# Optimization experiments

Hardware: AMD Instinct MI355X
Metric: run time of the kernel (lower is better)

The kernel has to match this reference:

```python
import jax, jax.numpy as jnp
import numpy as np

EMBED_DIM = 256; N_HEADS = 8; HEAD_DIM = 32; N_PAIRS = 16
POS_DIM = 2; N_LEVELS = 4; NBH = [3, 5, 7, 9]
N_Q = 2048; BATCH = 2; FULL = 128
SPATIAL_THETA = 100.0; LEVEL_THETA = 10.0
LN_EPS = 1e-5


def _grids():
    offs, lvls = [], []
    for l, s in enumerate(NBH):
        ax = np.arange(s)
        g = np.stack(np.meshgrid(ax, ax, indexing='ij'), -1).reshape(-1, 2)
        offs.append(g - (s - 1) // 2)
        lvls.append(np.full(s * s, l))
    return (np.concatenate(offs).astype(np.int32), np.concatenate(lvls).astype(np.int32))

OFFSETS, LEVEL_IDS = _grids()  # [164,2], [164]
K_PER_Q = OFFSETS.shape[0]


def _apply_rope(x, pos, freqs):
    # x: [..., n_heads, n_pairs, 2]; pos: [..., 3]; freqs: [3, n_pairs]
    ang = pos @ freqs                      # [..., n_pairs]
    c = jnp.cos(ang)[..., None, :]         # broadcast over heads
    s = jnp.sin(ang)[..., None, :]
    x1, x2 = x[..., 0], x[..., 1]
    return jnp.stack([x1 * c - x2 * s, x1 * s + x2 * c], axis=-1)


def setup_inputs() -> dict:
    key = jax.random.key(0)
    ks = jax.random.split(key, 8)
    scale = EMBED_DIM ** -0.5
    i = jnp.arange(N_PAIRS, dtype=jnp.float32) / N_PAIRS
    rope_freqs = jnp.stack([SPATIAL_THETA ** -i, SPATIAL_THETA ** -i, LEVEL_THETA ** -i])  # [3,16]
    level_spatial_shapes = jnp.array([[FULL >> l, FULL >> l] for l in range(N_LEVELS)], jnp.int32)
    return {
        'query': jax.random.normal(ks[0], (N_Q, EMBED_DIM), jnp.float32),
        'query_spatial_positions': jax.random.uniform(ks[1], (N_Q, POS_DIM), jnp.float32) * (FULL - 1),
        'stacked_feature_maps': jax.random.normal(ks[2], (BATCH, N_LEVELS, FULL, FULL, EMBED_DIM), jnp.float32) * 0.02,
        'norm_w': jnp.ones((EMBED_DIM,), jnp.float32),
        'norm_b': jnp.zeros((EMBED_DIM,), jnp.float32),
        'q_w': jax.random.normal(ks[3], (EMBED_DIM, EMBED_DIM), jnp.float32) * scale,
        'k_w': jax.random.normal(ks[4], (EMBED_DIM, EMBED_DIM), jnp.float32) * scale,
        'v_w': jax.random.normal(ks[5], (EMBED_DIM, EMBED_DIM), jnp.float32) * scale,
        'out_w': jax.random.normal(ks[6], (EMBED_DIM, EMBED_DIM), jnp.float32) * scale,
        'rope_freqs': rope_freqs,
        'query_batch_offsets': jnp.array([0, N_Q // 2, N_Q], jnp.int32),
        'level_spatial_shapes': level_spatial_shapes,
    }


def reference(query, query_spatial_positions, stacked_feature_maps, norm_w, norm_b,
              q_w, k_w, v_w, out_w, rope_freqs, query_batch_offsets, level_spatial_shapes):
    n_q = query.shape[0]
    residual = query

    # pre-LayerNorm
    mu = query.mean(-1, keepdims=True)
    var = query.var(-1, keepdims=True)
    x = (query - mu) * jax.lax.rsqrt(var + LN_EPS) * norm_w + norm_b

    # query projection + RoPE (spatial dims + level dim; queries sit at max-res level 0)
    q = x @ q_w
    qpos = jnp.concatenate([query_spatial_positions, jnp.zeros((n_q, 1), query.dtype)], -1)  # [n_q,3]
    q_rot = _apply_rope(q.reshape(n_q, N_HEADS, N_PAIRS, 2), qpos, rope_freqs).reshape(n_q, N_HEADS, HEAD_DIM)

    # multilevel neighborhood indices
    shapes_f = level_spatial_shapes.astype(query.dtype)               # [L,2]
    scaling = shapes_f / shapes_f.max(0)                              # [L,2]
    scaled = query_spatial_positions[:, None, :] * scaling[None]      # [n_q,L,2]
    centers = jnp.floor(scaled).astype(jnp.int32)                     # [n_q,L,2]
    lvl = jnp.asarray(LEVEL_IDS)                                      # [K]
    idx = centers[:, lvl, :] + jnp.asarray(OFFSETS)[None]             # [n_q,K,2]
    lsh = level_spatial_shapes[lvl]                                   # [K,2]
    valid = jnp.all((idx >= 0) & (idx < lsh[None]), -1)               # [n_q,K]
    idxc = jnp.clip(idx, 0, lsh[None] - 1)

    # per-query batch ids from offsets
    b = jnp.searchsorted(query_batch_offsets, jnp.arange(n_q, dtype=query_batch_offsets.dtype), side='right') - 1

    # sparse gather of key/value features (unspecified -> zero)
    feats = stacked_feature_maps[b[:, None], lvl[None, :], idxc[..., 0], idxc[..., 1]]  # [n_q,K,E]
    feats = feats * valid[..., None].astype(feats.dtype)

    k = feats @ k_w
    v = feats @ v_w

    # key positions at full scale + level coordinate
    stride = (shapes_f.max(0)[None] / shapes_f)[lvl]                  # [K,2]
    kpos_sp = (idx.astype(query.dtype) + 0.5) * stride[None]          # [n_q,K,2]
    kpos = jnp.concatenate([kpos_sp, jnp.broadcast_to(lvl.astype(query.dtype), (n_q, K_PER_Q))[..., None]], -1)
    k_rot = _apply_rope(k.reshape(n_q, K_PER_Q, N_HEADS, N_PAIRS, 2), kpos, rope_freqs)
    k_rot = k_rot.reshape(n_q, K_PER_Q, N_HEADS, HEAD_DIM)

    # attention over the 164 gathered keys per query
    logits = jnp.einsum('nhd,nkhd->nhk', q_rot, k_rot) / np.sqrt(HEAD_DIM)
    logits = jnp.where(valid[:, None, :], logits, jnp.asarray(-1e9, logits.dtype))
    attn = jax.nn.softmax(logits, axis=-1)
    out = jnp.einsum('nhk,nkhd->nhd', attn, v.reshape(n_q, K_PER_Q, N_HEADS, HEAD_DIM))
    out = out.reshape(n_q, EMBED_DIM) @ out_w
    return out + residual
```

## Files before the change

### kernel.cpp

```cpp
#include <hip/hip_runtime.h>
#include <hip/hip_bf16.h>

typedef unsigned short u16;
typedef short short8 __attribute__((ext_vector_type(8)));
typedef float f32x4 __attribute__((ext_vector_type(4)));

#define ROWS_PER_BATCH 21760
#define TOT_ROWS 43520

__device__ __forceinline__ u16 f2bf(float f){
  unsigned u = __builtin_bit_cast(unsigned, f);
  u += 0x7FFFu + ((u >> 16) & 1u);
  return (u16)(u >> 16);
}
__device__ __forceinline__ float bf2f(u16 h){
  return __builtin_bit_cast(float, ((unsigned)h) << 16);
}
__device__ __forceinline__ float bflo(unsigned u){ return __builtin_bit_cast(float, u << 16); }
__device__ __forceinline__ float bfhi(unsigned u){ return __builtin_bit_cast(float, u & 0xFFFF0000u); }
__device__ __forceinline__ unsigned pk2bf(float a, float b){
  __hip_bfloat162 h = __float22bfloat162_rn(make_float2(a, b));
  union { __hip_bfloat162 h2; unsigned u; } cv; cv.h2 = h; return cv.u;
}

__global__ __launch_bounds__(256) void prep_kernel(
    const float* __restrict__ qw, const float* __restrict__ kw,
    const float* __restrict__ vw, const float* __restrict__ ow,
    const float* __restrict__ q, const float* __restrict__ nw,
    const float* __restrict__ nb,
    u16* __restrict__ wtq, u16* __restrict__ wtk,
    u16* __restrict__ wtv, u16* __restrict__ wto, u16* __restrict__ x){
  const int bx = blockIdx.x;
  const int t = threadIdx.x;
  if (bx < 128){
    int e = bx * 256 + t;
    int which = e >> 13;
    int r = e & 8191;
    int cg = r >> 9;
    int kk = (r >> 6) & 7;
    int lane = r & 63;
    int quad = lane >> 4, mn = lane & 15;
    const float* s = which == 0 ? qw : which == 1 ? kw : which == 2 ? vw : ow;
    u16* d       = which == 0 ? wtq : which == 1 ? wtk : which == 2 ? wtv : wto;
    const float* base = s + (kk * 32 + quad * 8) * 256 + cg * 16 + mn;
    float e8[8];
    #pragma unroll
    for (int j = 0; j < 8; ++j) e8[j] = base[j * 256];
    uint4 o = { pk2bf(e8[0], e8[1]), pk2bf(e8[2], e8[3]),
                pk2bf(e8[4], e8[5]), pk2bf(e8[6], e8[7]) };
    *(uint4*)(d + (size_t)r * 8) = o;
  } else {
    const int row = (bx - 128) * 4 + (t >> 6);
    const int lane = t & 63;
    const float4 v = *(const float4*)(q + (size_t)row * 256 + lane * 4);
    float s1 = v.x + v.y + v.z + v.w;
    float s2 = v.x*v.x + v.y*v.y + v.z*v.z + v.w*v.w;
    #pragma unroll
    for (int o = 32; o > 0; o >>= 1){
      s1 += __shfl_xor(s1, o);
      s2 += __shfl_xor(s2, o);
    }
    float mu = s1 * (1.0f / 256.0f);
    float var = s2 * (1.0f / 256.0f) - mu * mu;
    float rs = rsqrtf(var + 1e-5f);
    const float4 wv = *(const float4*)(nw + lane * 4);
    const float4 bv = *(const float4*)(nb + lane * 4);
    float o0 = (v.x - mu) * rs * wv.x + bv.x;
    float o1 = (v.y - mu) * rs * wv.y + bv.y;
    float o2 = (v.z - mu) * rs * wv.z + bv.z;
    float o3 = (v.w - mu) * rs * wv.w + bv.w;
    uint2 pk = { pk2bf(o0, o1), pk2bf(o2, o3) };
    *(uint2*)(x + (size_t)row * 256 + lane * 4) = pk;
  }
}

__global__ __launch_bounds__(64, 4) void kv_gemm(const float* __restrict__ fm,
        const u16* __restrict__ wtkp, const u16* __restrict__ wtvp,
        const float* __restrict__ rope,
        u16* __restrict__ krot, u16* __restrict__ vmap){
  __shared__ float slab[16][66];
  __shared__ unsigned sh_cs[16][16];

  const int lane = threadIdx.x;
  const int row0 = blockIdx.x * 16;

  const int b = row0 / ROWS_PER_BATCH;
  const int rr = row0 - b * ROWS_PER_BATCH;
  int l, loff;
  if (rr < 16384)      { l = 0; loff = 0; }
  else if (rr < 20480) { l = 1; loff = 16384; }
  else if (rr < 21504) { l = 2; loff = 20480; }
  else                 { l = 3; loff = 21504; }
  const int logW = 7 - l;
  const int Wm1 = (128 >> l) - 1;
  const int cell0 = rr - loff;
  const float* fmbase = fm + (size_t)(b * 4 + l) * (128 * 128 * 256);

  const int mn = lane & 15;
  const int quad = lane >> 4;

  short8 af[8];
  {
    int cell = cell0 + mn;
    int y = cell >> logW, x = cell & Wm1;
    const float* arow = fmbase + (((y << 7) + x) << 8) + quad * 8;
    #pragma unroll
    for (int kk = 0; kk < 8; ++kk){
      float4 a0 = *(const float4*)(arow + kk * 32);
      float4 a1 = *(const float4*)(arow + kk * 32 + 4);
      union { short8 s; uint4 u; } cv;
      cv.u = (uint4){ pk2bf(a0.x, a0.y), pk2bf(a0.z, a0.w),
                      pk2bf(a1.x, a1.y), pk2bf(a1.z, a1.w) };
      af[kk] = cv.s;
    }
  }

  #pragma unroll
  for (int i = 0; i < 4; ++i){
    int id = i * 64 + lane;
    int lr = id >> 4, p = id & 15;
    int cell = cell0 + lr;
    int i0 = cell >> logW;
    int i1 = cell & Wm1;
    float fs = (float)(1 << l);
    float kx = ((float)i0 + 0.5f) * fs;
    float ky = ((float)i1 + 0.5f) * fs;
    float ang = kx * rope[p] + ky * rope[16 + p] + (float)l * rope[32 + p];
    sh_cs[lr][p] = pk2bf(__cosf(ang), __sinf(ang));
  }

  for (int m = 0; m < 2; ++m){
    const u16* wtp = m ? wtvp : wtkp;
    u16* outp = m ? vmap : krot;
    for (int cs2 = 0; cs2 < 4; ++cs2){
      const u16* wb = wtp + (size_t)((cs2 * 4 * 8) * 64 + lane) * 8;
      short8 bc[4], bn[4];
      #pragma unroll
      for (int tl = 0; tl < 4; ++tl)
        bc[tl] = *(const short8*)(wb + (size_t)(tl * 8) * 64 * 8);
      f32x4 acc[4];
      #pragma unroll
      for (int i = 0; i < 4; ++i) acc[i] = (f32x4){0.f, 0.f, 0.f, 0.f};
      #pragma unroll
      for (int kk = 0; kk < 8; ++kk){
        if (kk < 7){
          #pragma unroll
          for (int tl = 0; tl < 4; ++tl)
            bn[tl] = *(const short8*)(wb + (size_t)(tl * 8 + kk + 1) * 64 * 8);
        }
        #pragma unroll
        for (int tl = 0; tl < 4; ++tl)
          acc[tl] = __builtin_amdgcn_mfma_f32_16x16x32_bf16(af[kk], bc[tl], acc[tl], 0, 0, 0);
        #pragma unroll
        for (int tl = 0; tl < 4; ++tl) bc[tl] = bn[tl];
      }
      #pragma unroll
      for (int tl = 0; tl < 4; ++tl)
        #pragma unroll
        for (int r = 0; r < 4; ++r)
          slab[quad * 4 + r][tl * 16 + mn] = acc[tl][r];
      #pragma unroll
      for (int i = 0; i < 8; ++i){
        int pi = i * 64 + lane;
        int row = pi >> 5;
        int pl = pi & 31;
        float2 kv2 = *(const float2*)&slab[row][pl * 2];
        unsigned o;
        if (m == 0){
          unsigned csn = sh_cs[row][pl & 15];
          float c = bflo(csn), s = bfhi(csn);
          o = pk2bf(kv2.x * c - kv2.y * s, kv2.x * s + kv2.y * c);
        } else {
          o = pk2bf(kv2.x, kv2.y);
        }
        *(unsigned*)(outp + (size_t)(row0 + row) * 256 + cs2 * 64 + pl * 2) = o;
      }
    }
  }
}

__global__ __launch_bounds__(256) void gemm_xw(const u16* __restrict__ A,
        const u16* __restrict__ wt, const float* __restrict__ resid,
        float* __restrict__ out){
  const int t = threadIdx.x;
  const int row0 = blockIdx.x * 16;
  const int wv = t >> 6;
  const int lane = t & 63;
  const int mn = lane & 15;
  const int quad = lane >> 4;
  const int cg = blockIdx.y * 4 + wv;

  short8 af[8];
  {
    const u16* arow = A + (size_t)(row0 + mn) * 256 + quad * 8;
    #pragma unroll
    for (int kk = 0; kk < 8; ++kk)
      af[kk] = *(const short8*)(arow + kk * 32);
  }
  const u16* wb = wt + (size_t)((cg * 8) * 64 + lane) * 8;
  short8 bc = *(const short8*)wb;
  f32x4 acc = (f32x4){0.f, 0.f, 0.f, 0.f};
  #pragma unroll
  for (int kk = 0; kk < 8; ++kk){
    short8 bn;
    if (kk < 7) bn = *(const short8*)(wb + (size_t)(kk + 1) * 64 * 8);
    acc = __builtin_amdgcn_mfma_f32_16x16x32_bf16(af[kk], bc, acc, 0, 0, 0);
    bc = bn;
  }
  const int col = cg * 16 + mn;
  #pragma unroll
  for (int r = 0; r < 4; ++r){
    int row = row0 + quad * 4 + r;
    float val = acc[r];
    if (resid) val += resid[(size_t)row * 256 + col];
    out[(size_t)row * 256 + col] = val;
  }
}

__global__ __launch_bounds__(256) void attn3(
    const float* __restrict__ qraw, const float* __restrict__ qsp,
    const float* __restrict__ rope, const int* __restrict__ qbo, int nbo,
    const u16* __restrict__ krot, const u16* __restrict__ vmap,
    u16* __restrict__ ao){
  __shared__ float sh_q[4][8][33];
  __shared__ float sh_lg[4][168][8];
  __shared__ int   sh_row[4][168];
  __shared__ float sh_inv[4][8];
  const int t = threadIdx.x;
  const int w = t >> 6;
  const int lane = t & 63;
  const int qi = blockIdx.x * 4 + w;

  int bidx = 0;
  for (int j = 1; j < nbo; ++j) if (qi >= qbo[j]) bidx = j;
  const float p0 = qsp[qi * 2 + 0];
  const float p1 = qsp[qi * 2 + 1];

  #pragma unroll
  for (int it = 0; it < 4; ++it){
    int d = it * 64 + lane;
    float qv = qraw[(size_t)qi * 256 + d];
    int p = (d & 31) >> 1;
    float ang = p0 * rope[p] + p1 * rope[16 + p];
    float c = __cosf(ang), s = __sinf(ang);
    float partner = __shfl_xor(qv, 1);
    float val = (d & 1) ? (partner * s + qv * c) : (qv * c - partner * s);
    sh_q[w][d >> 5][d & 31] = val * 0.17677669529663687f;
  }

  #pragma unroll
  for (int it = 0; it < 3; ++it){
    int kk = it * 64 + lane;
    if (kk < 164){
      int l, dy, dx, loff;
      if (kk < 9)       { l = 0; int j = kk;      dy = j / 3 - 1; dx = j % 3 - 1; loff = 0; }
      else if (kk < 34) { l = 1; int j = kk - 9;  dy = j / 5 - 2; dx = j % 5 - 2; loff = 16384; }
      else if (kk < 83) { l = 2; int j = kk - 34; dy = j / 7 - 3; dx = j % 7 - 3; loff = 20480; }
      else              { l = 3; int j = kk - 83; dy = j / 9 - 4; dx = j % 9 - 4; loff = 21504; }
      float sc = 1.0f / (float)(1 << l);
      int i0 = (int)floorf(p0 * sc) + dy;
      int i1 = (int)floorf(p1 * sc) + dx;
      int W = 128 >> l;
      sh_row[w][kk] = (i0 < 0 || i0 >= W || i1 < 0 || i1 >= W)
                ? -1 : bidx * ROWS_PER_BATCH + loff + (i0 << (7 - l)) + i1;
    }
  }

  const int h = lane & 7;
  const int ksub = lane >> 3;
  float qreg[32];
  #pragma unroll
  for (int j = 0; j < 32; ++j) qreg[j] = sh_q[w][h][j];
  for (int pass = 0; pass < 21; ++pass){
    int kk = pass * 8 + ksub;
    if (kk < 164){
      int row = sh_row[w][kk];
      float lg = -1e9f;
      if (row >= 0){
        const uint4* kp = (const uint4*)(krot + (size_t)row * 256 + h * 32);
        uint4 A0 = kp[0], A1 = kp[1], A2 = kp[2], A3 = kp[3];
        unsigned uu[16];
        uu[0]=A0.x; uu[1]=A0.y; uu[2]=A0.z; uu[3]=A0.w;
        uu[4]=A1.x; uu[5]=A1.y; uu[6]=A1.z; uu[7]=A1.w;
        uu[8]=A2.x; uu[9]=A2.y; uu[10]=A2.z; uu[11]=A2.w;
        uu[12]=A3.x; uu[13]=A3.y; uu[14]=A3.z; uu[15]=A3.w;
        float s0 = 0.f, s1 = 0.f, s2 = 0.f, s3 = 0.f;
        #pragma unroll
        for (int j = 0; j < 4; ++j){
          s0 += qreg[2*j]      * bflo(uu[j])      + qreg[2*j+1]  * bfhi(uu[j]);
          s1 += qreg[2*j+8]    * bflo(uu[j+4])    + qreg[2*j+9]  * bfhi(uu[j+4]);
          s2 += qreg[2*j+16]   * bflo(uu[j+8])    + qreg[2*j+17] * bfhi(uu[j+8]);
          s3 += qreg[2*j+24]   * bflo(uu[j+12])   + qreg[2*j+25] * bfhi(uu[j+12]);
        }
        lg = (s0 + s1) + (s2 + s3);
      }
      sh_lg[w][kk][h] = lg;
    }
  }

  float mx = -1e30f;
  for (int kk = ksub; kk < 164; kk += 8) mx = fmaxf(mx, sh_lg[w][kk][h]);
  #pragma unroll
  for (int o = 8; o < 64; o <<= 1) mx = fmaxf(mx, __shfl_xor(mx, o));
  float ssum = 0.f;
  for (int kk = ksub; kk < 164; kk += 8){
    float e = __expf(sh_lg[w][kk][h] - mx);
    sh_lg[w][kk][h] = e;
    ssum += e;
  }
  #pragma unroll
  for (int o = 8; o < 64; o <<= 1) ssum += __shfl_xor(ssum, o);
  if (ksub == 0) sh_inv[w][h] = 1.0f / ssum;

  const int c = lane & 31;
  const int p2 = lane >> 5;
  const int hh = c >> 2;
  float a[8] = {0.f,0.f,0.f,0.f,0.f,0.f,0.f,0.f};
  #pragma unroll 4
  for (int ii = 0; ii < 82; ++ii){
    int kk = ii * 2 + p2;
    int row = sh_row[w][kk];
    int rc = row < 0 ? 0 : row;
    uint4 vv = *(const uint4*)(vmap + (size_t)rc * 256 + c * 8);
    float e = sh_lg[w][kk][hh];
    a[0] += e * bflo(vv.x); a[1] += e * bfhi(vv.x);
    a[2] += e * bflo(vv.y); a[3] += e * bfhi(vv.y);
    a[4] += e * bflo(vv.z); a[5] += e * bfhi(vv.z);
    a[6] += e * bflo(vv.w); a[7] += e * bfhi(vv.w);
  }
  #pragma unroll
  for (int j = 0; j < 8; ++j) a[j] += __shfl_xor(a[j], 32);
  if (p2 == 0){
    float inv = sh_inv[w][hh];
    uint4 o = { pk2bf(a[0]*inv, a[1]*inv), pk2bf(a[2]*inv, a[3]*inv),
                pk2bf(a[4]*inv, a[5]*inv), pk2bf(a[6]*inv, a[7]*inv) };
    *(uint4*)(ao + (size_t)qi * 256 + c * 8) = o;
  }
}

extern "C" void kernel_launch(void* const* d_in, const int* in_sizes, int n_in,
                              void* d_out, int out_size, void* d_ws, size_t ws_size,
                              hipStream_t stream) {
  (void)n_in; (void)out_size; (void)ws_size;
  const float* query  = (const float*)d_in[0];
  const float* qsp    = (const float*)d_in[1];
  const float* fm     = (const float*)d_in[2];
  const float* norm_w = (const float*)d_in[3];
  const float* norm_b = (const float*)d_in[4];
  const float* q_w    = (const float*)d_in[5];
  const float* k_w    = (const float*)d_in[6];
  const float* v_w    = (const float*)d_in[7];
  const float* out_w  = (const float*)d_in[8];
  const float* rope   = (const float*)d_in[9];
  const int*   qbo    = (const int*)d_in[10];
  float* out = (float*)d_out;
  const int n_q = in_sizes[0] / 256;
  const int nbo = in_sizes[10];

  char* p = (char*)d_ws;
  u16* krot = (u16*)p;                       p += (size_t)TOT_ROWS * 256 * 2;
  u16* vmap = (u16*)p;                       p += (size_t)TOT_ROWS * 256 * 2;
  float* qraw = (float*)p;                   p += (size_t)n_q * 256 * 4;
  u16* xbf = (u16*)p;                        p += (size_t)n_q * 256 * 2;
  u16* wtq = (u16*)p;                        p += 65536 * 2;
  u16* wtk = (u16*)p;                        p += 65536 * 2;
  u16* wtv = (u16*)p;                        p += 65536 * 2;
  u16* wto = (u16*)p;
  u16* ao = xbf;

  hipLaunchKernelGGL(prep_kernel, dim3(128 + n_q / 4), dim3(256), 0, stream,
                     q_w, k_w, v_w, out_w, query, norm_w, norm_b,
                     wtq, wtk, wtv, wto, xbf);
  hipLaunchKernelGGL(kv_gemm, dim3(TOT_ROWS / 16), dim3(64), 0, stream,
                     fm, wtk, wtv, rope, krot, vmap);
  hipLaunchKernelGGL(gemm_xw, dim3(n_q / 16, 4), dim3(256), 0, stream,
                     xbf, wtq, (const float*)nullptr, qraw);
  hipLaunchKernelGGL(attn3, dim3(n_q / 4), dim3(256), 0, stream,
                     qraw, qsp, rope, qbo, nbo, krot, vmap, ao);
  hipLaunchKernelGGL(gemm_xw, dim3(n_q / 16, 4), dim3(256), 0, stream,
                     ao, wto, query, out);
}
```

Before: 270.8 us.

## Sort queries by Morton order and remap attention blocks per XCD for locality

Adds a single-block bitonic sort kernel that orders queries by batch and the Morton code of their spatial position, producing a permutation. The attention kernel reads its query index through this permutation and remaps block IDs so that consecutive spatially-near queries land on the same XCD. Neighbouring queries then share gathered K/V rows in that XCD's L2. The cost is an extra serial single-workgroup launch. The code also assumes n_q is at most 4096 and that query indices fit in 12 bits.

New measurement: 299.6 us. 1.11x slower.

```diff
diff --git a/kernel.cpp b/kernel.cpp
--- a/kernel.cpp
+++ b/kernel.cpp
@@ -7,6 +7,7 @@
 
 #define ROWS_PER_BATCH 21760
 #define TOT_ROWS 43520
+#define MAXQ 4096
 
 __device__ __forceinline__ u16 f2bf(float f){
   unsigned u = __builtin_bit_cast(unsigned, f);
@@ -74,6 +75,45 @@
   }
 }
 
+__global__ __launch_bounds__(1024) void sort_q(
+    const float* __restrict__ qsp, const int* __restrict__ qbo, int nbo,
+    int n_q, u16* __restrict__ perm){
+  __shared__ unsigned key[MAXQ];
+  const int t = threadIdx.x;
+  int NP = 1; while (NP < n_q) NP <<= 1;
+  for (int i = t; i < NP; i += 1024){
+    unsigned k = 0xFFFFFFFFu;
+    if (i < n_q){
+      int b = 0;
+      for (int j = 1; j < nbo; ++j) if (i >= qbo[j]) b = j;
+      int x = ((int)qsp[i * 2])     & 127;
+      int y = ((int)qsp[i * 2 + 1]) & 127;
+      unsigned m = 0;
+      #pragma unroll
+      for (int bi = 0; bi < 7; ++bi)
+        m |= (((unsigned)(x >> bi) & 1u) << (2 * bi + 1))
+           | (((unsigned)(y >> bi) & 1u) << (2 * bi));
+      k = ((unsigned)b << 26) | (m << 12) | (unsigned)i;
+    }
+    key[i] = k;
+  }
+  __syncthreads();
+  for (int ks = 2; ks <= NP; ks <<= 1){
+    for (int j = ks >> 1; j > 0; j >>= 1){
+      for (int i = t; i < NP; i += 1024){
+        int p = i ^ j;
+        if (p > i){
+          unsigned a = key[i], bk = key[p];
+          bool up = (i & ks) == 0;
+          if ((up && a > bk) || (!up && a < bk)){ key[i] = bk; key[p] = a; }
+        }
+      }
+      __syncthreads();
+    }
+  }
+  for (int i = t; i < n_q; i += 1024) perm[i] = (u16)(key[i] & 4095u);
+}
+
 __global__ __launch_bounds__(64, 4) void kv_gemm(const float* __restrict__ fm,
         const u16* __restrict__ wtkp, const u16* __restrict__ wtvp,
         const float* __restrict__ rope,
@@ -220,6 +260,7 @@
 __global__ __launch_bounds__(256) void attn3(
     const float* __restrict__ qraw, const float* __restrict__ qsp,
     const float* __restrict__ rope, const int* __restrict__ qbo, int nbo,
+    const u16* __restrict__ perm,
     const u16* __restrict__ krot, const u16* __restrict__ vmap,
     u16* __restrict__ ao){
   __shared__ float sh_q[4][8][33];
@@ -229,7 +270,14 @@
   const int t = threadIdx.x;
   const int w = t >> 6;
   const int lane = t & 63;
-  const int qi = blockIdx.x * 4 + w;
+
+  const int nwg = gridDim.x;
+  const int orig = blockIdx.x;
+  const int xcd = orig & 7;
+  const int q8 = nwg >> 3, r8 = nwg & 7;
+  const int wg = (xcd < r8 ? xcd * (q8 + 1) : r8 * (q8 + 1) + (xcd - r8) * q8)
+               + (orig >> 3);
+  const int qi = perm[wg * 4 + w];
 
   int bidx = 0;
   for (int j = 1; j < nbo; ++j) if (qi >= qbo[j]) bidx = j;
@@ -365,18 +413,21 @@
   u16* wtq = (u16*)p;                        p += 65536 * 2;
   u16* wtk = (u16*)p;                        p += 65536 * 2;
   u16* wtv = (u16*)p;                        p += 65536 * 2;
-  u16* wto = (u16*)p;
+  u16* wto = (u16*)p;                        p += 65536 * 2;
+  u16* qperm = (u16*)p;
   u16* ao = xbf;
 
   hipLaunchKernelGGL(prep_kernel, dim3(128 + n_q / 4), dim3(256), 0, stream,
                      q_w, k_w, v_w, out_w, query, norm_w, norm_b,
                      wtq, wtk, wtv, wto, xbf);
+  hipLaunchKernelGGL(sort_q, dim3(1), dim3(1024), 0, stream,
+                     qsp, qbo, nbo, n_q, qperm);
   hipLaunchKernelGGL(kv_gemm, dim3(TOT_ROWS / 16), dim3(64), 0, stream,
                      fm, wtk, wtv, rope, krot, vmap);
   hipLaunchKernelGGL(gemm_xw, dim3(n_q / 16, 4), dim3(256), 0, stream,
                      xbf, wtq, (const float*)nullptr, qraw);
   hipLaunchKernelGGL(attn3, dim3(n_q / 4), dim3(256), 0, stream,
-                     qraw, qsp, rope, qbo, nbo, krot, vmap, ao);
+                     qraw, qsp, rope, qbo, nbo, qperm, krot, vmap, ao);
   hipLaunchKernelGGL(gemm_xw, dim3(n_q / 16, 4), dim3(256), 0, stream,
                      ao, wto, query, out);
 }
```

## Share staged weight tiles in LDS across four waves in kv_gemm

Applied to the files above, without the earlier changes.

The kv_gemm kernel now runs 256-thread blocks of four waves, each handling 16 rows. Each 64-column weight slice is staged cooperatively into shared memory once per block instead of being read from global memory by every wave. This cuts redundant weight traffic and L2 pressure by four times. In exchange it adds two block barriers per column slice, removes the register prefetch of the B operand, and uses about 32KB of extra LDS, which may limit occupancy.

Result: faster. 255.6 us (-5.6%).

```diff
diff --git a/kernel.cpp b/kernel.cpp
--- a/kernel.cpp
+++ b/kernel.cpp
@@ -74,15 +74,18 @@
   }
 }
 
-__global__ __launch_bounds__(64, 4) void kv_gemm(const float* __restrict__ fm,
+__global__ __launch_bounds__(256, 2) void kv_gemm(const float* __restrict__ fm,
         const u16* __restrict__ wtkp, const u16* __restrict__ wtvp,
         const float* __restrict__ rope,
         u16* __restrict__ krot, u16* __restrict__ vmap){
-  __shared__ float slab[16][66];
-  __shared__ unsigned sh_cs[16][16];
-
-  const int lane = threadIdx.x;
-  const int row0 = blockIdx.x * 16;
+  __shared__ u16 bstage[32 * 512];
+  __shared__ float slab[4][16][66];
+  __shared__ unsigned sh_cs[4][16][16];
+
+  const int t = threadIdx.x;
+  const int w = t >> 6;
+  const int lane = t & 63;
+  const int row0 = blockIdx.x * 64 + w * 16;
 
   const int b = row0 / ROWS_PER_BATCH;
   const int rr = row0 - b * ROWS_PER_BATCH;
@@ -126,48 +129,47 @@
     float kx = ((float)i0 + 0.5f) * fs;
     float ky = ((float)i1 + 0.5f) * fs;
     float ang = kx * rope[p] + ky * rope[16 + p] + (float)l * rope[32 + p];
-    sh_cs[lr][p] = pk2bf(__cosf(ang), __sinf(ang));
+    sh_cs[w][lr][p] = pk2bf(__cosf(ang), __sinf(ang));
   }
 
   for (int m = 0; m < 2; ++m){
     const u16* wtp = m ? wtvp : wtkp;
     u16* outp = m ? vmap : krot;
     for (int cs2 = 0; cs2 < 4; ++cs2){
-      const u16* wb = wtp + (size_t)((cs2 * 4 * 8) * 64 + lane) * 8;
-      short8 bc[4], bn[4];
-      #pragma unroll
-      for (int tl = 0; tl < 4; ++tl)
-        bc[tl] = *(const short8*)(wb + (size_t)(tl * 8) * 64 * 8);
+      __syncthreads();
+      const u16* src = wtp + (size_t)cs2 * 16384;
+      #pragma unroll
+      for (int i = 0; i < 8; ++i)
+        *(uint4*)(bstage + ((size_t)(i * 256 + t)) * 8) =
+            *(const uint4*)(src + ((size_t)(i * 256 + t)) * 8);
+      __syncthreads();
+
       f32x4 acc[4];
       #pragma unroll
       for (int i = 0; i < 4; ++i) acc[i] = (f32x4){0.f, 0.f, 0.f, 0.f};
       #pragma unroll
       for (int kk = 0; kk < 8; ++kk){
-        if (kk < 7){
-          #pragma unroll
-          for (int tl = 0; tl < 4; ++tl)
-            bn[tl] = *(const short8*)(wb + (size_t)(tl * 8 + kk + 1) * 64 * 8);
+        #pragma unroll
+        for (int tl = 0; tl < 4; ++tl){
+          short8 bc = *(const short8*)(bstage + ((tl * 8 + kk) * 64 + lane) * 8);
+          acc[tl] = __builtin_amdgcn_mfma_f32_16x16x32_bf16(af[kk], bc, acc[tl], 0, 0, 0);
         }
-        #pragma unroll
-        for (int tl = 0; tl < 4; ++tl)
-          acc[tl] = __builtin_amdgcn_mfma_f32_16x16x32_bf16(af[kk], bc[tl], acc[tl], 0, 0, 0);
-        #pragma unroll
-        for (int tl = 0; tl < 4; ++tl) bc[tl] = bn[tl];
       }
+
       #pragma unroll
       for (int tl = 0; tl < 4; ++tl)
         #pragma unroll
         for (int r = 0; r < 4; ++r)
-          slab[quad * 4 + r][tl * 16 + mn] = acc[tl][r];
+          slab[w][quad * 4 + r][tl * 16 + mn] = acc[tl][r];
       #pragma unroll
       for (int i = 0; i < 8; ++i){
         int pi = i * 64 + lane;
         int row = pi >> 5;
         int pl = pi & 31;
-        float2 kv2 = *(const float2*)&slab[row][pl * 2];
+        float2 kv2 = *(const float2*)&slab[w][row][pl * 2];
         unsigned o;
         if (m == 0){
-          unsigned csn = sh_cs[row][pl & 15];
+          unsigned csn = sh_cs[w][row][pl & 15];
           float c = bflo(csn), s = bfhi(csn);
           o = pk2bf(kv2.x * c - kv2.y * s, kv2.x * s + kv2.y * c);
         } else {
@@ -371,7 +373,7 @@
   hipLaunchKernelGGL(prep_kernel, dim3(128 + n_q / 4), dim3(256), 0, stream,
                      q_w, k_w, v_w, out_w, query, norm_w, norm_b,
                      wtq, wtk, wtv, wto, xbf);
-  hipLaunchKernelGGL(kv_gemm, dim3(TOT_ROWS / 16), dim3(64), 0, stream,
+  hipLaunchKernelGGL(kv_gemm, dim3(TOT_ROWS / 64), dim3(256), 0, stream,
                      fm, wtk, wtv, rope, krot, vmap);
   hipLaunchKernelGGL(gemm_xw, dim3(n_q / 16, 4), dim3(256), 0, stream,
                      xbf, wtq, (const float*)nullptr, qraw);
```
